# Kernel optimization log

Measured on AMD Instinct MI355X. Metric: run time of the kernel, lower is better.

The kernel has to match this reference:

```python
import jax, jax.numpy as jnp
import numpy as np

B, T, IN = 64, 64, 64      # batch, seq_len, input feature dim
C = 256                    # controller_size
N = 1024                   # memory_locations
MV = 64                    # memory_vector_size
OUT = 64                   # output_size
SHIFTS = (-1, 0, 1)        # maximum_shifts = 3 -> shifts -1,0,+1
EPS = 1e-8


def _glorot(key, shape):
    lim = np.sqrt(6.0 / (shape[0] + shape[1]))
    return jax.random.uniform(key, shape, jnp.float32, -lim, lim)


def setup_inputs() -> dict:
    key = jax.random.key(0)
    ks = jax.random.split(key, 8)
    x = jax.random.normal(ks[0], (B, T, IN), jnp.float32)
    # controller FC: input = concat(x_t, r_{t-1})
    Wc = _glorot(ks[1], (IN + MV, C)); bc = jnp.zeros((C,), jnp.float32)
    # read head emits k(MV), beta(1), g(1), s(3), gamma(1)
    Wr = _glorot(ks[2], (C, MV + 6)); br = jnp.zeros((MV + 6,), jnp.float32)
    # write head emits k, beta, g, s, gamma, e(MV), a(MV)
    Ww = _glorot(ks[3], (C, 3 * MV + 6)); bw = jnp.zeros((3 * MV + 6,), jnp.float32)
    # final FC: input = concat(controller_out, r_t)
    Wf = _glorot(ks[4], (C + MV, OUT)); bf = jnp.zeros((OUT,), jnp.float32)
    # state biases, as in NTM.__init__
    r_bias = 0.5 * jax.random.truncated_normal(ks[5], -2.0, 2.0, (1, MV)).astype(jnp.float32)
    w_bias = jax.nn.softmax(jax.random.normal(ks[6], (1, N), jnp.float32), axis=-1)
    M_bias = jnp.full((1, N, MV), 1e-6, jnp.float32)
    return {"x": x, "Wc": Wc, "bc": bc, "Wr": Wr, "br": br, "Ww": Ww, "bw": bw,
            "Wf": Wf, "bf": bf, "r_bias": r_bias, "w_bias": w_bias, "M_bias": M_bias}


def _head_params(h):
    # h: [B, MV+6] raw head projections
    k = jnp.tanh(h[:, :MV])                               # key [B,MV]
    beta = jax.nn.softplus(h[:, MV:MV + 1])               # key strength > 0
    g = jax.nn.sigmoid(h[:, MV + 1:MV + 2])               # interpolation gate
    s = jax.nn.softmax(h[:, MV + 2:MV + 5], axis=-1)      # shift weights [B,3]
    gamma = 1.0 + jax.nn.softplus(h[:, MV + 5:MV + 6])    # sharpening >= 1
    return k, beta, g, s, gamma


def _address(w_prev, M, k, beta, g, s, gamma):
    # content addressing: cosine similarity between key and memory rows
    dot = jnp.einsum('bnm,bm->bn', M, k)
    norms = jnp.linalg.norm(M, axis=-1) * jnp.linalg.norm(k, axis=-1, keepdims=True)
    w_c = jax.nn.softmax(beta * dot / (norms + EPS), axis=-1)
    # interpolation with previous weights
    w_g = g * w_c + (1.0 - g) * w_prev
    # circular convolution shift
    shifted = jnp.stack([jnp.roll(w_g, sh, axis=1) for sh in SHIFTS], axis=-1)  # [B,N,3]
    w_s = jnp.einsum('bns,bs->bn', shifted, s)
    # sharpening
    w_pow = (w_s + EPS) ** gamma
    return w_pow / jnp.sum(w_pow, axis=-1, keepdims=True)


def reference(x, Wc, bc, Wr, br, Ww, bw, Wf, bf, r_bias, w_bias, M_bias):
    b = x.shape[0]
    r0 = jnp.tile(r_bias, (b, 1))          # [B,MV]
    w0 = jnp.tile(w_bias, (b, 1))          # [B,N]
    M0 = jnp.tile(M_bias, (b, 1, 1))       # [B,N,MV]

    def step(carry, x_t):
        r, w, M = carry
        c = jnp.tanh(jnp.concatenate([x_t, r], axis=1) @ Wc + bc)   # controller [B,C]
        # write head: address, then erase + add memory update
        hw = c @ Ww + bw
        k, beta, g, s, gamma = _head_params(hw[:, :MV + 6])
        e = jax.nn.sigmoid(hw[:, MV + 6:2 * MV + 6])   # erase vector
        a = jnp.tanh(hw[:, 2 * MV + 6:])               # add vector
        w_w = _address(w, M, k, beta, g, s, gamma)     # [B,N]
        M = M * (1.0 - w_w[:, :, None] * e[:, None, :]) + w_w[:, :, None] * a[:, None, :]
        # read head: address (using write head's weights as previous), then read
        hr = c @ Wr + br
        w_r = _address(w_w, M, *_head_params(hr))
        r = jnp.einsum('bn,bnm->bm', w_r, M)           # read vector [B,MV]
        out = jax.nn.sigmoid(jnp.concatenate([c, r], axis=1) @ Wf + bf)
        return (r, w_r, M), out

    _, ys = jax.lax.scan(step, (r0, w0, M0), jnp.transpose(x, (1, 0, 2)))
    return jnp.transpose(ys, (1, 0, 2))  # [B,T,OUT]
```

## Files before the change

### kernel.cpp

```cpp
#include <hip/hip_runtime.h>
#include <hip/hip_bf16.h>
#include <math.h>


constexpr int kB  = 64;
constexpr int kT  = 64;
constexpr int kIN = 64;
constexpr int kC  = 256;
constexpr int kN  = 1024;
constexpr int kMV = 64;
constexpr int kOUT = 64;
constexpr int kHW = 198;
constexpr int kHR = 70;
constexpr int kHO = kHW + kHR;
constexpr int kHCP = 320;
constexpr int NT  = 512;
constexpr int NW  = NT / 64;
constexpr float kEPS = 1e-8f;

constexpr int kPWc = 0;
constexpr int kPHc = kPWc + kC * 128;
constexpr int kPWf = kPHc + kC * kHCP;
constexpr int kPTotal = kPWf + kOUT * (kC + kMV);
constexpr size_t kWsPack = 256 + (size_t)kPTotal * 4;
constexpr int kCpreElems = kB * kT * kC;
constexpr size_t kWsFull = kWsPack + (size_t)kCpreElems * 4;

__device__ __forceinline__ float ldf(const float* p, int i) { return p[i]; }
__device__ __forceinline__ float ldf(const __hip_bfloat16* p, int i) { return __bfloat162float(p[i]); }
__device__ __forceinline__ void stf(float* p, int i, float v) { p[i] = v; }
__device__ __forceinline__ void stf(__hip_bfloat16* p, int i, float v) { p[i] = __float2bfloat16(v); }

__device__ __forceinline__ void ld8(const __hip_bfloat16* p, float* f) {
  uint4 u = *reinterpret_cast<const uint4*>(p);
  f[0] = __uint_as_float(u.x << 16); f[1] = __uint_as_float(u.x & 0xffff0000u);
  f[2] = __uint_as_float(u.y << 16); f[3] = __uint_as_float(u.y & 0xffff0000u);
  f[4] = __uint_as_float(u.z << 16); f[5] = __uint_as_float(u.z & 0xffff0000u);
  f[6] = __uint_as_float(u.w << 16); f[7] = __uint_as_float(u.w & 0xffff0000u);
}
__device__ __forceinline__ void ld8(const float* p, float* f) {
  float4 a = reinterpret_cast<const float4*>(p)[0];
  float4 b = reinterpret_cast<const float4*>(p)[1];
  f[0] = a.x; f[1] = a.y; f[2] = a.z; f[3] = a.w;
  f[4] = b.x; f[5] = b.y; f[6] = b.z; f[7] = b.w;
}

__device__ __forceinline__ float fexp(float v) { return __expf(v); }
__device__ __forceinline__ float sigmoidf_(float v) {
  return __fdividef(1.f, 1.f + __expf(-v));
}
__device__ __forceinline__ float softplusf_(float v) {
  return v > 20.f ? v : __logf(1.f + __expf(v));
}
__device__ __forceinline__ float ftanh(float v) {
  float a = fminf(fabsf(v), 15.f);
  float e = __expf(2.f * a);
  float t = 1.f - __fdividef(2.f, e + 1.f);
  return v < 0.f ? -t : t;
}

__device__ __forceinline__ float wsum(float v) {
  v += __shfl_xor(v, 32); v += __shfl_xor(v, 16); v += __shfl_xor(v, 8);
  v += __shfl_xor(v, 4);  v += __shfl_xor(v, 2);  v += __shfl_xor(v, 1);
  return v;
}

template <typename TD>
__device__ __forceinline__ float dot64(const TD* row, const float* vec) {
  float a0 = 0.f, a1 = 0.f, a2 = 0.f, a3 = 0.f;
  #pragma unroll
  for (int q = 0; q < 8; ++q) {
    float f[8]; ld8(row + 8 * q, f);
    float4 va = *(const float4*)&vec[8 * q];
    float4 vb = *(const float4*)&vec[8 * q + 4];
    a0 = fmaf(va.x, f[0], a0); a1 = fmaf(va.y, f[1], a1);
    a2 = fmaf(va.z, f[2], a2); a3 = fmaf(va.w, f[3], a3);
    a0 = fmaf(vb.x, f[4], a0); a1 = fmaf(vb.y, f[5], a1);
    a2 = fmaf(vb.z, f[6], a2); a3 = fmaf(vb.w, f[7], a3);
  }
  return (a0 + a1) + (a2 + a3);
}

struct alignas(16) Smem {
  float M1s[16 * 512 * 4];
  float partA[1280];
  float E[kN];
  float WP[kN];
  float c[kC];
  float r[kMV];
  float k[kMV], kr[kMV], e[kMV], a[kMV];
  float bcS[kC], bwS[kHW], brS[kHR], bfS[kOUT];
  float red[2][NW];
  float scal[16];
};
static_assert(sizeof(Smem) <= 160 * 1024, "LDS budget");

__device__ __forceinline__ int m1idx(int blk, int row) { return (blk * 512 + row) * 4; }

__global__ void detect_dtype(const void* wb, int* flag) {
  const unsigned short* u = (const unsigned short*)wb;
  int lane = threadIdx.x;
  float s = 0.f;
  for (int i = lane; i < kN; i += 64)
    s += __uint_as_float(((unsigned int)u[i]) << 16);
  s = wsum(s);
  if (lane == 0 && blockIdx.x == 0)
    *flag = (s > 0.75f && s < 1.25f) ? 1 : 0;
}

template <typename TD, int WANT>
__global__ void repack_w(const TD* __restrict__ Wc, const TD* __restrict__ Ww,
                         const TD* __restrict__ Wr, const TD* __restrict__ Wf,
                         TD* __restrict__ pk, const int* __restrict__ flag) {
  if (*flag != WANT) return;
  for (int idx = blockIdx.x * blockDim.x + threadIdx.x; idx < kPTotal;
       idx += gridDim.x * blockDim.x) {
    TD v = (TD)0.0f;
    if (idx < kPHc) {
      int r = idx, j = r >> 7, i = r & 127;
      v = Wc[i * kC + j];
    } else if (idx < kPWf) {
      int r = idx - kPHc, i = r / kHCP, o = r - i * kHCP;
      if (o < kHW) v = Ww[i * kHW + o];
      else if (o < kHO) v = Wr[i * kHR + (o - kHW)];
    } else {
      int r = idx - kPWf, j = r / 320, i = r % 320;
      v = Wf[i * kOUT + j];
    }
    pk[idx] = v;
  }
}

template <typename TD, int WANT>
__global__ void cpre_kernel(const TD* __restrict__ x, const TD* __restrict__ bc,
                            const TD* __restrict__ pk, float* __restrict__ cpre,
                            const int* __restrict__ flag) {
  if (*flag != WANT) return;
  const int bt = blockIdx.x;
  const int tid = threadIdx.x;
  __shared__ float xs[kIN];
  if (tid < kIN) xs[tid] = ldf(x, (size_t)bt * kIN + tid);
  __syncthreads();
  const TD* row = pk + kPWc + tid * 128;
  float s = ldf(bc, tid) + dot64(row, xs);
  cpre[(size_t)bt * kC + tid] = s;
}

template <typename TD, int WANT, int MODE>
__global__ __launch_bounds__(NT, 1) void ntm_fused(
    const TD* __restrict__ x,
    const TD* __restrict__ Wc, const TD* __restrict__ bc,
    const TD* __restrict__ Wr, const TD* __restrict__ br,
    const TD* __restrict__ Ww, const TD* __restrict__ bw,
    const TD* __restrict__ Wf, const TD* __restrict__ bf,
    const TD* __restrict__ r_bias, const TD* __restrict__ w_bias,
    const TD* __restrict__ M_bias,
    const TD* __restrict__ pk, const float* __restrict__ cpre,
    TD* __restrict__ out, const int* __restrict__ flag) {
  if (*flag != WANT) return;
  __shared__ Smem sm;
  const int tid  = threadIdx.x;
  const int b    = blockIdx.x;
  const int lane = tid & 63;
  const int wid  = tid >> 6;

  if (tid < kC)  sm.bcS[tid] = ldf(bc, tid);
  if (tid < kHW) sm.bwS[tid] = ldf(bw, tid);
  if (tid < kHR) sm.brS[tid] = ldf(br, tid);
  if (tid < kOUT) sm.bfS[tid] = ldf(bf, tid);
  if (tid < kMV) sm.r[tid] = ldf(r_bias, tid);

  float M0[kMV];
  float n2_0 = 0.f, n2_1 = 0.f;
  #pragma unroll
  for (int jb = 0; jb < kMV; jb += 8) {
    float f0[8], f1[8];
    ld8(M_bias + (size_t)tid * kMV + jb, f0);
    ld8(M_bias + (size_t)(tid + NT) * kMV + jb, f1);
    #pragma unroll
    for (int u = 0; u < 8; ++u) {
      M0[jb + u] = f0[u];
      n2_0 = fmaf(f0[u], f0[u], n2_0);
      n2_1 = fmaf(f1[u], f1[u], n2_1);
    }
    *(float4*)&sm.M1s[m1idx(jb >> 2, tid)] = make_float4(f1[0], f1[1], f1[2], f1[3]);
    *(float4*)&sm.M1s[m1idx((jb >> 2) + 1, tid)] = make_float4(f1[4], f1[5], f1[6], f1[7]);
  }
  float wp0 = ldf(w_bias, tid);
  float wp1 = ldf(w_bias, tid + NT);
  __syncthreads();

  #pragma unroll 1
  for (int t = 0; t < kT; ++t) {
    if constexpr (MODE == 2) {
      if (tid < 256) {
        const int si = lane >> 3;
        const int g  = (wid << 3) + (lane & 7);
        const int obase = g * 8;
        float acc[8] = {0.f, 0.f, 0.f, 0.f, 0.f, 0.f, 0.f, 0.f};
        #pragma unroll
        for (int q = 0; q < 8; ++q) {
          int i = (q << 3) + si;
          float rv = sm.r[i];
          float f[8]; ld8(Wc + (kIN + i) * kC + obase, f);
          #pragma unroll
          for (int v = 0; v < 8; ++v) acc[v] = fmaf(rv, f[v], acc[v]);
        }
        #pragma unroll
        for (int v = 0; v < 8; ++v) {
          acc[v] += __shfl_xor(acc[v], 8);
          acc[v] += __shfl_xor(acc[v], 16);
          acc[v] += __shfl_xor(acc[v], 32);
        }
        if (si == 0) {
          const float* cp = &cpre[((size_t)b * kT + t) * kC + obase];
          float4 ca = *(const float4*)cp;
          float4 cb = *(const float4*)(cp + 4);
          sm.c[obase + 0] = ftanh(ca.x + acc[0]);
          sm.c[obase + 1] = ftanh(ca.y + acc[1]);
          sm.c[obase + 2] = ftanh(ca.z + acc[2]);
          sm.c[obase + 3] = ftanh(ca.w + acc[3]);
          sm.c[obase + 4] = ftanh(cb.x + acc[4]);
          sm.c[obase + 5] = ftanh(cb.y + acc[5]);
          sm.c[obase + 6] = ftanh(cb.z + acc[6]);
          sm.c[obase + 7] = ftanh(cb.w + acc[7]);
        }
      } else if (tid < 320 && t > 0) {
        const int j = tid - 256;
        float s = sm.bfS[j] + sm.partA[512 + j] + sm.partA[576 + j];
        s += dot64(pk + kPWf + j * (kC + kMV) + kC, sm.r);
        stf(out, ((size_t)b * kT + (t - 1)) * kOUT + j, sigmoidf_(s));
      }
    } else {
      if (tid < kC) {
        float s;
        if constexpr (MODE == 1) {
          s = sm.bcS[tid];
          const TD* xrow = x + ((size_t)b * kT + t) * kIN;
          const TD* row = pk + kPWc + tid * 128;
          #pragma unroll
          for (int q = 0; q < 8; ++q) {
            float f[8], xv[8];
            ld8(row + 8 * q, f); ld8(xrow + 8 * q, xv);
            #pragma unroll
            for (int u = 0; u < 8; ++u) s = fmaf(xv[u], f[u], s);
          }
          s += dot64(pk + kPWc + tid * 128 + 64, sm.r);
        } else {
          s = sm.bcS[tid];
          for (int i = 0; i < kIN; ++i)
            s = fmaf(ldf(x, ((size_t)b * kT + t) * kIN + i), ldf(Wc, i * kC + tid), s);
          for (int i = 0; i < kMV; ++i)
            s = fmaf(sm.r[i], ldf(Wc, (kIN + i) * kC + tid), s);
        }
        sm.c[tid] = ftanh(s);
      } else if (tid < 320 && t > 0) {
        const int j = tid - 256;
        float s = sm.bfS[j] + sm.partA[512 + j] + sm.partA[576 + j];
        if constexpr (MODE >= 1) {
          s += dot64(pk + kPWf + j * (kC + kMV) + kC, sm.r);
        } else {
          for (int i = 0; i < kMV; ++i)
            s = fmaf(sm.r[i], ldf(Wf, (kC + i) * kOUT + j), s);
        }
        stf(out, ((size_t)b * kT + (t - 1)) * kOUT + j, sigmoidf_(s));
      }
    }
    __syncthreads();

    if constexpr (MODE >= 1) {
      if (wid < 5) {
        const int si = lane >> 3;
        const int g  = (wid << 3) + (lane & 7);
        const int obase = g * 8;
        float acc[8] = {0.f, 0.f, 0.f, 0.f, 0.f, 0.f, 0.f, 0.f};
        #pragma unroll 4
        for (int q = 0; q < 32; ++q) {
          int i = (q << 3) + si;
          float cv = sm.c[i];
          float f[8]; ld8(pk + kPHc + i * kHCP + obase, f);
          #pragma unroll
          for (int v = 0; v < 8; ++v) acc[v] = fmaf(cv, f[v], acc[v]);
        }
        #pragma unroll
        for (int v = 0; v < 8; ++v) {
          acc[v] += __shfl_xor(acc[v], 8);
          acc[v] += __shfl_xor(acc[v], 16);
          acc[v] += __shfl_xor(acc[v], 32);
        }
        if (si == 0 && obase < kHO) {
          #pragma unroll
          for (int v = 0; v < 8; ++v)
            if (obase + v < kHO) sm.partA[obase + v] = acc[v];
        }
      }
    } else {
      if (tid < kHO) {
        float a0 = 0.f;
        for (int i = 0; i < kC; ++i) {
          float wv = (tid < kHW) ? ldf(Ww, i * kHW + tid)
                                 : ldf(Wr, i * kHR + (tid - kHW));
          a0 = fmaf(sm.c[i], wv, a0);
        }
        sm.partA[tid] = a0;
      }
    }
    __syncthreads();

    if (wid == 0) {
      float kv = ftanh(sm.partA[lane] + sm.bwS[lane]);
      sm.k[lane] = kv;
      float s = wsum(kv * kv);
      if (lane == 0) sm.scal[6] = sqrtf(s);
    } else if (wid == 1) {
      sm.e[lane] = sigmoidf_(sm.partA[70 + lane] + sm.bwS[70 + lane]);
    } else if (wid == 2) {
      sm.a[lane] = ftanh(sm.partA[134 + lane] + sm.bwS[134 + lane]);
    } else if (wid == 3) {
      float kv = ftanh(sm.partA[kHW + lane] + sm.brS[lane]);
      sm.kr[lane] = kv;
      float s = wsum(kv * kv);
      if (lane == 0) sm.scal[14] = sqrtf(s);
    } else if (wid == 4 || wid == 5) {
      const int si = lane >> 3;
      const int g  = lane & 7;
      const int obase = g * 8;
      const int ibase = (wid - 4) * 128;
      float acc[8] = {0.f, 0.f, 0.f, 0.f, 0.f, 0.f, 0.f, 0.f};
      #pragma unroll 4
      for (int q = 0; q < 16; ++q) {
        int i = ibase + (q << 3) + si;
        float cv = sm.c[i];
        float f[8]; ld8(Wf + i * kOUT + obase, f);
        #pragma unroll
        for (int v = 0; v < 8; ++v) acc[v] = fmaf(cv, f[v], acc[v]);
      }
      #pragma unroll
      for (int v = 0; v < 8; ++v) {
        acc[v] += __shfl_xor(acc[v], 8);
        acc[v] += __shfl_xor(acc[v], 16);
        acc[v] += __shfl_xor(acc[v], 32);
      }
      if (si == 0) {
        *(float4*)&sm.partA[512 + (wid - 4) * 64 + obase] =
            make_float4(acc[0], acc[1], acc[2], acc[3]);
        *(float4*)&sm.partA[512 + (wid - 4) * 64 + obase + 4] =
            make_float4(acc[4], acc[5], acc[6], acc[7]);
      }
    }
    __syncthreads();

    float ww0, ww1, gW, s0W, s1W, s2W, gammaW;
    float e0W, e1W, p0W, p1W;
    {
      float beta = softplusf_(sm.partA[64] + sm.bwS[64]);
      gW = sigmoidf_(sm.partA[65] + sm.bwS[65]);
      gammaW = 1.f + softplusf_(sm.partA[69] + sm.bwS[69]);
      float a0 = sm.partA[66] + sm.bwS[66];
      float a1 = sm.partA[67] + sm.bwS[67];
      float a2 = sm.partA[68] + sm.bwS[68];
      float mx = fmaxf(a0, fmaxf(a1, a2));
      float ex0 = fexp(a0 - mx), ex1 = fexp(a1 - mx), ex2 = fexp(a2 - mx);
      float dd = __fdividef(1.f, ex0 + ex1 + ex2);
      s0W = ex0 * dd; s1W = ex1 * dd; s2W = ex2 * dd;
      float kn = sm.scal[6];
      float d0a = 0.f, d0b = 0.f, d1a = 0.f, d1b = 0.f;
      #pragma unroll
      for (int bq = 0; bq < 16; ++bq) {
        float4 kv = *(const float4*)&sm.k[bq * 4];
        d0a = fmaf(M0[bq * 4],     kv.x, d0a);
        d0b = fmaf(M0[bq * 4 + 1], kv.y, d0b);
        d0a = fmaf(M0[bq * 4 + 2], kv.z, d0a);
        d0b = fmaf(M0[bq * 4 + 3], kv.w, d0b);
        float4 mv = *(const float4*)&sm.M1s[m1idx(bq, tid)];
        d1a = fmaf(mv.x, kv.x, d1a); d1b = fmaf(mv.y, kv.y, d1b);
        d1a = fmaf(mv.z, kv.z, d1a); d1b = fmaf(mv.w, kv.w, d1b);
      }
      float d0 = d0a + d0b, d1 = d1a + d1b;
      float sim0 = fminf(beta * d0 / (sqrtf(n2_0) * kn + kEPS), 80.f);
      float sim1 = fminf(beta * d1 / (sqrtf(n2_1) * kn + kEPS), 80.f);
      e0W = fexp(sim0); e1W = fexp(sim1);
      sm.E[tid] = e0W; sm.E[tid + NT] = e1W;
      sm.WP[tid] = wp0; sm.WP[tid + NT] = wp1;
      float sv = wsum(e0W + e1W);
      if (lane == 0) sm.red[0][wid] = sv;
    }
    __syncthreads();

    {
      float gsum = 0.f;
      #pragma unroll
      for (int i = 0; i < NW; ++i) gsum += sm.red[0][i];
      float inv = __fdividef(1.f, gsum);
      float wg0 = fmaf(gW, fmaf(e0W, inv, -wp0), wp0);
      float wg1 = fmaf(gW, fmaf(e1W, inv, -wp1), wp1);
      int np = (tid + 1) & (kN - 1), nm = (tid + kN - 1) & (kN - 1);
      float wgp = fmaf(gW, fmaf(sm.E[np], inv, -sm.WP[np]), sm.WP[np]);
      float wgm = fmaf(gW, fmaf(sm.E[nm], inv, -sm.WP[nm]), sm.WP[nm]);
      float ws0 = s0W * wgp + s1W * wg0 + s2W * wgm;
      int npb = (tid + NT + 1) & (kN - 1), nmb = (tid + NT - 1) & (kN - 1);
      float wgpb = fmaf(gW, fmaf(sm.E[npb], inv, -sm.WP[npb]), sm.WP[npb]);
      float wgmb = fmaf(gW, fmaf(sm.E[nmb], inv, -sm.WP[nmb]), sm.WP[nmb]);
      float ws1 = s0W * wgpb + s1W * wg1 + s2W * wgmb;
      p0W = fexp(gammaW * __logf(ws0 + kEPS));
      p1W = fexp(gammaW * __logf(ws1 + kEPS));
      float pv = wsum(p0W + p1W);
      if (lane == 0) sm.red[1][wid] = pv;
    }
    __syncthreads();
    {
      float psum = 0.f;
      #pragma unroll
      for (int i = 0; i < NW; ++i) psum += sm.red[1][i];
      float ipn = __fdividef(1.f, psum);
      ww0 = p0W * ipn; ww1 = p1W * ipn;
    }

    float gR, s0R, s1R, s2R, gammaR;
    float e0R, e1R, p0R, p1R;
    float dr0 = 0.f, dr1 = 0.f, nn0 = 0.f, nn1 = 0.f;
    {
      #pragma unroll
      for (int bq = 0; bq < 16; ++bq) {
        float4 ev = *(const float4*)&sm.e[bq * 4];
        float4 av = *(const float4*)&sm.a[bq * 4];
        float4 kv = *(const float4*)&sm.kr[bq * 4];
        {
          float m = fmaf(ww0, fmaf(-ev.x, M0[bq * 4], av.x), M0[bq * 4]);
          M0[bq * 4] = m; dr0 = fmaf(m, kv.x, dr0); nn0 = fmaf(m, m, nn0);
        }
        {
          float m = fmaf(ww0, fmaf(-ev.y, M0[bq * 4 + 1], av.y), M0[bq * 4 + 1]);
          M0[bq * 4 + 1] = m; dr0 = fmaf(m, kv.y, dr0); nn0 = fmaf(m, m, nn0);
        }
        {
          float m = fmaf(ww0, fmaf(-ev.z, M0[bq * 4 + 2], av.z), M0[bq * 4 + 2]);
          M0[bq * 4 + 2] = m; dr0 = fmaf(m, kv.z, dr0); nn0 = fmaf(m, m, nn0);
        }
        {
          float m = fmaf(ww0, fmaf(-ev.w, M0[bq * 4 + 3], av.w), M0[bq * 4 + 3]);
          M0[bq * 4 + 3] = m; dr0 = fmaf(m, kv.w, dr0); nn0 = fmaf(m, m, nn0);
        }
        int fi = m1idx(bq, tid);
        float4 mv = *(const float4*)&sm.M1s[fi];
        float4 nm;
        nm.x = fmaf(ww1, fmaf(-ev.x, mv.x, av.x), mv.x);
        dr1 = fmaf(nm.x, kv.x, dr1); nn1 = fmaf(nm.x, nm.x, nn1);
        nm.y = fmaf(ww1, fmaf(-ev.y, mv.y, av.y), mv.y);
        dr1 = fmaf(nm.y, kv.y, dr1); nn1 = fmaf(nm.y, nm.y, nn1);
        nm.z = fmaf(ww1, fmaf(-ev.z, mv.z, av.z), mv.z);
        dr1 = fmaf(nm.z, kv.z, dr1); nn1 = fmaf(nm.z, nm.z, nn1);
        nm.w = fmaf(ww1, fmaf(-ev.w, mv.w, av.w), mv.w);
        dr1 = fmaf(nm.w, kv.w, dr1); nn1 = fmaf(nm.w, nm.w, nn1);
        *(float4*)&sm.M1s[fi] = nm;
      }
      float beta = softplusf_(sm.partA[kHW + 64] + sm.brS[64]);
      gR = sigmoidf_(sm.partA[kHW + 65] + sm.brS[65]);
      gammaR = 1.f + softplusf_(sm.partA[kHW + 69] + sm.brS[69]);
      float a0 = sm.partA[kHW + 66] + sm.brS[66];
      float a1 = sm.partA[kHW + 67] + sm.brS[67];
      float a2 = sm.partA[kHW + 68] + sm.brS[68];
      float mx = fmaxf(a0, fmaxf(a1, a2));
      float ex0 = fexp(a0 - mx), ex1 = fexp(a1 - mx), ex2 = fexp(a2 - mx);
      float dd = __fdividef(1.f, ex0 + ex1 + ex2);
      s0R = ex0 * dd; s1R = ex1 * dd; s2R = ex2 * dd;
      float kn = sm.scal[14];
      float sim0 = fminf(beta * dr0 / (sqrtf(nn0) * kn + kEPS), 80.f);
      float sim1 = fminf(beta * dr1 / (sqrtf(nn1) * kn + kEPS), 80.f);
      e0R = fexp(sim0); e1R = fexp(sim1);
      sm.E[tid] = e0R; sm.E[tid + NT] = e1R;
      sm.WP[tid] = ww0; sm.WP[tid + NT] = ww1;
      float sv = wsum(e0R + e1R);
      if (lane == 0) sm.red[0][wid] = sv;
    }
    __syncthreads();

    {
      float gsum = 0.f;
      #pragma unroll
      for (int i = 0; i < NW; ++i) gsum += sm.red[0][i];
      float inv = __fdividef(1.f, gsum);
      float wg0 = fmaf(gR, fmaf(e0R, inv, -ww0), ww0);
      float wg1 = fmaf(gR, fmaf(e1R, inv, -ww1), ww1);
      int np = (tid + 1) & (kN - 1), nm = (tid + kN - 1) & (kN - 1);
      float wgp = fmaf(gR, fmaf(sm.E[np], inv, -sm.WP[np]), sm.WP[np]);
      float wgm = fmaf(gR, fmaf(sm.E[nm], inv, -sm.WP[nm]), sm.WP[nm]);
      float ws0 = s0R * wgp + s1R * wg0 + s2R * wgm;
      int npb = (tid + NT + 1) & (kN - 1), nmb = (tid + NT - 1) & (kN - 1);
      float wgpb = fmaf(gR, fmaf(sm.E[npb], inv, -sm.WP[npb]), sm.WP[npb]);
      float wgmb = fmaf(gR, fmaf(sm.E[nmb], inv, -sm.WP[nmb]), sm.WP[nmb]);
      float ws1 = s0R * wgpb + s1R * wg1 + s2R * wgmb;
      p0R = fexp(gammaR * __logf(ws0 + kEPS));
      p1R = fexp(gammaR * __logf(ws1 + kEPS));
      float pv = wsum(p0R + p1R);
      if (lane == 0) sm.red[1][wid] = pv;
      {
        float cur[16];
        const int b0 = lane & 1;
        #pragma unroll
        for (int qq = 0; qq < 8; ++qq) {
          float4 mv = *(const float4*)&sm.M1s[m1idx(qq, tid)];
          float v0 = fmaf(p0R, M0[4 * qq],     p1R * mv.x);
          float v1 = fmaf(p0R, M0[4 * qq + 1], p1R * mv.y);
          float keep = b0 ? v1 : v0, send = b0 ? v0 : v1;
          cur[2 * qq] = keep + __shfl_xor(send, 1);
          float v2 = fmaf(p0R, M0[4 * qq + 2], p1R * mv.z);
          float v3 = fmaf(p0R, M0[4 * qq + 3], p1R * mv.w);
          keep = b0 ? v3 : v2; send = b0 ? v2 : v3;
          cur[2 * qq + 1] = keep + __shfl_xor(send, 1);
        }
        #pragma unroll
        for (int st = 1; st < 5; ++st) {
          const int d = 1 << st;
          const int bb = (lane >> st) & 1;
          #pragma unroll
          for (int q = 0; q < (16 >> st); ++q) {
            float x0 = cur[2 * q], x1 = cur[2 * q + 1];
            float keep = bb ? x1 : x0, send = bb ? x0 : x1;
            cur[q] = keep + __shfl_xor(send, d);
          }
        }
        float tot = cur[0] + __shfl_xor(cur[0], 32);
        if (lane < 32) sm.partA[768 + wid * 64 + lane] = tot;
      }
      {
        float cur[16];
        const int b0 = lane & 1;
        #pragma unroll
        for (int qq = 0; qq < 8; ++qq) {
          float4 mv = *(const float4*)&sm.M1s[m1idx(8 + qq, tid)];
          float v0 = fmaf(p0R, M0[32 + 4 * qq],     p1R * mv.x);
          float v1 = fmaf(p0R, M0[32 + 4 * qq + 1], p1R * mv.y);
          float keep = b0 ? v1 : v0, send = b0 ? v0 : v1;
          cur[2 * qq] = keep + __shfl_xor(send, 1);
          float v2 = fmaf(p0R, M0[32 + 4 * qq + 2], p1R * mv.z);
          float v3 = fmaf(p0R, M0[32 + 4 * qq + 3], p1R * mv.w);
          keep = b0 ? v3 : v2; send = b0 ? v2 : v3;
          cur[2 * qq + 1] = keep + __shfl_xor(send, 1);
        }
        #pragma unroll
        for (int st = 1; st < 5; ++st) {
          const int d = 1 << st;
          const int bb = (lane >> st) & 1;
          #pragma unroll
          for (int q = 0; q < (16 >> st); ++q) {
            float x0 = cur[2 * q], x1 = cur[2 * q + 1];
            float keep = bb ? x1 : x0, send = bb ? x0 : x1;
            cur[q] = keep + __shfl_xor(send, d);
          }
        }
        float tot = cur[0] + __shfl_xor(cur[0], 32);
        if (lane < 32) sm.partA[768 + wid * 64 + 32 + lane] = tot;
      }
    }
    __syncthreads();

    {
      float psum = 0.f;
      #pragma unroll
      for (int i = 0; i < NW; ++i) psum += sm.red[1][i];
      float ipn = __fdividef(1.f, psum);
      wp0 = p0R * ipn; wp1 = p1R * ipn;
      n2_0 = nn0; n2_1 = nn1;
      if (tid < kMV) {
        float s = sm.partA[768 + tid];
        #pragma unroll
        for (int w = 1; w < NW; ++w) s += sm.partA[768 + w * 64 + tid];
        sm.r[tid] = s * ipn;
      }
    }
    __syncthreads();
  }

  if (tid >= 256 && tid < 320) {
    const int j = tid - 256;
    float s = sm.bfS[j] + sm.partA[512 + j] + sm.partA[576 + j];
    if constexpr (MODE >= 1) {
      s += dot64(pk + kPWf + j * (kC + kMV) + kC, sm.r);
    } else {
      for (int i = 0; i < kMV; ++i)
        s = fmaf(sm.r[i], ldf(Wf, (kC + i) * kOUT + j), s);
    }
    stf(out, ((size_t)b * kT + (kT - 1)) * kOUT + j, sigmoidf_(s));
  }
}

template <typename TD, int WANT, int MODE>
static void launch_variant(void* const* d_in, void* d_out, const int* flag,
                           const void* pk, const float* cpre, hipStream_t stream) {
  ntm_fused<TD, WANT, MODE><<<dim3(kB), dim3(NT), 0, stream>>>(
      (const TD*)d_in[0], (const TD*)d_in[1], (const TD*)d_in[2],
      (const TD*)d_in[3], (const TD*)d_in[4], (const TD*)d_in[5],
      (const TD*)d_in[6], (const TD*)d_in[7], (const TD*)d_in[8],
      (const TD*)d_in[9], (const TD*)d_in[10], (const TD*)d_in[11],
      (const TD*)pk, cpre, (TD*)d_out, flag);
}

extern "C" void kernel_launch(void* const* d_in, const int* in_sizes, int n_in,
                              void* d_out, int out_size, void* d_ws, size_t ws_size,
                              hipStream_t stream) {
  (void)in_sizes; (void)n_in; (void)out_size;
  int* flag = (int*)d_ws;
  detect_dtype<<<dim3(1), dim3(64), 0, stream>>>(d_in[10], flag);
  if (ws_size >= kWsPack) {
    void* pk = (void*)((char*)d_ws + 256);
    repack_w<__hip_bfloat16, 1><<<dim3(256), dim3(256), 0, stream>>>(
        (const __hip_bfloat16*)d_in[1], (const __hip_bfloat16*)d_in[5],
        (const __hip_bfloat16*)d_in[3], (const __hip_bfloat16*)d_in[7],
        (__hip_bfloat16*)pk, flag);
    repack_w<float, 0><<<dim3(256), dim3(256), 0, stream>>>(
        (const float*)d_in[1], (const float*)d_in[5],
        (const float*)d_in[3], (const float*)d_in[7],
        (float*)pk, flag);
    if (ws_size >= kWsFull) {
      float* cpre = (float*)((char*)d_ws + kWsPack);
      cpre_kernel<__hip_bfloat16, 1><<<dim3(kB * kT), dim3(kC), 0, stream>>>(
          (const __hip_bfloat16*)d_in[0], (const __hip_bfloat16*)d_in[2],
          (const __hip_bfloat16*)pk, cpre, flag);
      cpre_kernel<float, 0><<<dim3(kB * kT), dim3(kC), 0, stream>>>(
          (const float*)d_in[0], (const float*)d_in[2],
          (const float*)pk, cpre, flag);
      launch_variant<__hip_bfloat16, 1, 2>(d_in, d_out, flag, pk, cpre, stream);
      launch_variant<float, 0, 2>(d_in, d_out, flag, pk, cpre, stream);
    } else {
      launch_variant<__hip_bfloat16, 1, 1>(d_in, d_out, flag, pk, nullptr, stream);
      launch_variant<float, 0, 1>(d_in, d_out, flag, pk, nullptr, stream);
    }
  } else {
    launch_variant<__hip_bfloat16, 1, 0>(d_in, d_out, flag, nullptr, nullptr, stream);
    launch_variant<float, 0, 0>(d_in, d_out, flag, nullptr, nullptr, stream);
  }
}
```

Before: 1.010 ms.

## Repack weights as fp32 and move Wf controller projection into head-GEMM phase

The packed weight buffer is now always fp32 and gains two new row-major copies: the recurrent part of Wc and the controller part of Wf. The per-step recurrent controller matvec and the Wf·c projection read from these packed copies instead of the raw inputs. The Wf·c projection moves from two warps in a later phase to a single warp (wid 5) running alongside the head GEMM, which removes one partial-sum add. In exchange the packed buffer is larger, bf16 inputs are read at double the bytes, and one warp now does twice the Wf work.

Measured after the change: 979.7 us. 1.03x faster.

```diff
diff --git a/kernel.cpp b/kernel.cpp
--- a/kernel.cpp
+++ b/kernel.cpp
@@ -18,10 +18,12 @@
 constexpr int NW  = NT / 64;
 constexpr float kEPS = 1e-8f;
 
-constexpr int kPWc = 0;
-constexpr int kPHc = kPWc + kC * 128;
-constexpr int kPWf = kPHc + kC * kHCP;
-constexpr int kPTotal = kPWf + kOUT * (kC + kMV);
+constexpr int kPWcT = 0;
+constexpr int kPHc  = kPWcT + kC * 128;
+constexpr int kPWfT = kPHc + kC * kHCP;
+constexpr int kPWcR = kPWfT + kOUT * (kC + kMV);
+constexpr int kPWfR = kPWcR + kMV * kC;
+constexpr int kPTotal = kPWfR + kC * kOUT;
 constexpr size_t kWsPack = 256 + (size_t)kPTotal * 4;
 constexpr int kCpreElems = kB * kT * kC;
 constexpr size_t kWsFull = kWsPack + (size_t)kCpreElems * 4;
@@ -111,21 +113,27 @@
 template <typename TD, int WANT>
 __global__ void repack_w(const TD* __restrict__ Wc, const TD* __restrict__ Ww,
                          const TD* __restrict__ Wr, const TD* __restrict__ Wf,
-                         TD* __restrict__ pk, const int* __restrict__ flag) {
+                         float* __restrict__ pk, const int* __restrict__ flag) {
   if (*flag != WANT) return;
   for (int idx = blockIdx.x * blockDim.x + threadIdx.x; idx < kPTotal;
        idx += gridDim.x * blockDim.x) {
-    TD v = (TD)0.0f;
+    float v = 0.0f;
     if (idx < kPHc) {
       int r = idx, j = r >> 7, i = r & 127;
-      v = Wc[i * kC + j];
-    } else if (idx < kPWf) {
+      v = ldf(Wc, i * kC + j);
+    } else if (idx < kPWfT) {
       int r = idx - kPHc, i = r / kHCP, o = r - i * kHCP;
-      if (o < kHW) v = Ww[i * kHW + o];
-      else if (o < kHO) v = Wr[i * kHR + (o - kHW)];
+      if (o < kHW) v = ldf(Ww, i * kHW + o);
+      else if (o < kHO) v = ldf(Wr, i * kHR + (o - kHW));
+    } else if (idx < kPWcR) {
+      int r = idx - kPWfT, j = r / 320, i = r % 320;
+      v = ldf(Wf, i * kOUT + j);
+    } else if (idx < kPWfR) {
+      int r = idx - kPWcR, i = r >> 8, j = r & 255;
+      v = ldf(Wc, (kIN + i) * kC + j);
     } else {
-      int r = idx - kPWf, j = r / 320, i = r % 320;
-      v = Wf[i * kOUT + j];
+      int r = idx - kPWfR, i = r >> 6, j = r & 63;
+      v = ldf(Wf, i * kOUT + j);
     }
     pk[idx] = v;
   }
@@ -133,7 +141,7 @@
 
 template <typename TD, int WANT>
 __global__ void cpre_kernel(const TD* __restrict__ x, const TD* __restrict__ bc,
-                            const TD* __restrict__ pk, float* __restrict__ cpre,
+                            const float* __restrict__ pk, float* __restrict__ cpre,
                             const int* __restrict__ flag) {
   if (*flag != WANT) return;
   const int bt = blockIdx.x;
@@ -141,7 +149,7 @@
   __shared__ float xs[kIN];
   if (tid < kIN) xs[tid] = ldf(x, (size_t)bt * kIN + tid);
   __syncthreads();
-  const TD* row = pk + kPWc + tid * 128;
+  const float* row = pk + kPWcT + tid * 128;
   float s = ldf(bc, tid) + dot64(row, xs);
   cpre[(size_t)bt * kC + tid] = s;
 }
@@ -155,7 +163,7 @@
     const TD* __restrict__ Wf, const TD* __restrict__ bf,
     const TD* __restrict__ r_bias, const TD* __restrict__ w_bias,
     const TD* __restrict__ M_bias,
-    const TD* __restrict__ pk, const float* __restrict__ cpre,
+    const float* __restrict__ pk, const float* __restrict__ cpre,
     TD* __restrict__ out, const int* __restrict__ flag) {
   if (*flag != WANT) return;
   __shared__ Smem sm;
@@ -202,7 +210,7 @@
         for (int q = 0; q < 8; ++q) {
           int i = (q << 3) + si;
           float rv = sm.r[i];
-          float f[8]; ld8(Wc + (kIN + i) * kC + obase, f);
+          float f[8]; ld8(pk + kPWcR + i * kC + obase, f);
           #pragma unroll
           for (int v = 0; v < 8; ++v) acc[v] = fmaf(rv, f[v], acc[v]);
         }
@@ -227,8 +235,8 @@
         }
       } else if (tid < 320 && t > 0) {
         const int j = tid - 256;
-        float s = sm.bfS[j] + sm.partA[512 + j] + sm.partA[576 + j];
-        s += dot64(pk + kPWf + j * (kC + kMV) + kC, sm.r);
+        float s = sm.bfS[j] + sm.partA[512 + j];
+        s += dot64(pk + kPWfT + j * (kC + kMV) + kC, sm.r);
         stf(out, ((size_t)b * kT + (t - 1)) * kOUT + j, sigmoidf_(s));
       }
     } else {
@@ -237,7 +245,7 @@
         if constexpr (MODE == 1) {
           s = sm.bcS[tid];
           const TD* xrow = x + ((size_t)b * kT + t) * kIN;
-          const TD* row = pk + kPWc + tid * 128;
+          const float* row = pk + kPWcT + tid * 128;
           #pragma unroll
           for (int q = 0; q < 8; ++q) {
             float f[8], xv[8];
@@ -245,7 +253,7 @@
             #pragma unroll
             for (int u = 0; u < 8; ++u) s = fmaf(xv[u], f[u], s);
           }
-          s += dot64(pk + kPWc + tid * 128 + 64, sm.r);
+          s += dot64(pk + kPWcT + tid * 128 + 64, sm.r);
         } else {
           s = sm.bcS[tid];
           for (int i = 0; i < kIN; ++i)
@@ -256,9 +264,9 @@
         sm.c[tid] = ftanh(s);
       } else if (tid < 320 && t > 0) {
         const int j = tid - 256;
-        float s = sm.bfS[j] + sm.partA[512 + j] + sm.partA[576 + j];
-        if constexpr (MODE >= 1) {
-          s += dot64(pk + kPWf + j * (kC + kMV) + kC, sm.r);
+        float s = sm.bfS[j] + sm.partA[512 + j];
+        if constexpr (MODE == 1) {
+          s += dot64(pk + kPWfT + j * (kC + kMV) + kC, sm.r);
         } else {
           for (int i = 0; i < kMV; ++i)
             s = fmaf(sm.r[i], ldf(Wf, (kC + i) * kOUT + j), s);
@@ -293,6 +301,31 @@
           for (int v = 0; v < 8; ++v)
             if (obase + v < kHO) sm.partA[obase + v] = acc[v];
         }
+      } else if (wid == 5) {
+        const int si = lane >> 3;
+        const int g  = lane & 7;
+        const int obase = g * 8;
+        float acc[8] = {0.f, 0.f, 0.f, 0.f, 0.f, 0.f, 0.f, 0.f};
+        #pragma unroll 4
+        for (int q = 0; q < 32; ++q) {
+          int i = (q << 3) + si;
+          float cv = sm.c[i];
+          float f[8]; ld8(pk + kPWfR + i * kOUT + obase, f);
+          #pragma unroll
+          for (int v = 0; v < 8; ++v) acc[v] = fmaf(cv, f[v], acc[v]);
+        }
+        #pragma unroll
+        for (int v = 0; v < 8; ++v) {
+          acc[v] += __shfl_xor(acc[v], 8);
+          acc[v] += __shfl_xor(acc[v], 16);
+          acc[v] += __shfl_xor(acc[v], 32);
+        }
+        if (si == 0) {
+          *(float4*)&sm.partA[512 + obase] =
+              make_float4(acc[0], acc[1], acc[2], acc[3]);
+          *(float4*)&sm.partA[512 + obase + 4] =
+              make_float4(acc[4], acc[5], acc[6], acc[7]);
+        }
       }
     } else {
       if (tid < kHO) {
@@ -303,6 +336,28 @@
           a0 = fmaf(sm.c[i], wv, a0);
         }
         sm.partA[tid] = a0;
+      } else if (wid == 5) {
+        const int si = lane >> 3;
+        const int g  = lane & 7;
+        const int obase = g * 8;
+        float acc[8] = {0.f, 0.f, 0.f, 0.f, 0.f, 0.f, 0.f, 0.f};
+        for (int q = 0; q < 32; ++q) {
+          int i = (q << 3) + si;
+          float cv = sm.c[i];
+          #pragma unroll
+          for (int v = 0; v < 8; ++v)
+            acc[v] = fmaf(cv, ldf(Wf, i * kOUT + obase + v), acc[v]);
+        }
+        #pragma unroll
+        for (int v = 0; v < 8; ++v) {
+          acc[v] += __shfl_xor(acc[v], 8);
+          acc[v] += __shfl_xor(acc[v], 16);
+          acc[v] += __shfl_xor(acc[v], 32);
+        }
+        if (si == 0) {
+          #pragma unroll
+          for (int v = 0; v < 8; ++v) sm.partA[512 + obase + v] = acc[v];
+        }
       }
     }
     __syncthreads();
@@ -321,32 +376,6 @@
       sm.kr[lane] = kv;
       float s = wsum(kv * kv);
       if (lane == 0) sm.scal[14] = sqrtf(s);
-    } else if (wid == 4 || wid == 5) {
-      const int si = lane >> 3;
-      const int g  = lane & 7;
-      const int obase = g * 8;
-      const int ibase = (wid - 4) * 128;
-      float acc[8] = {0.f, 0.f, 0.f, 0.f, 0.f, 0.f, 0.f, 0.f};
-      #pragma unroll 4
-      for (int q = 0; q < 16; ++q) {
-        int i = ibase + (q << 3) + si;
-        float cv = sm.c[i];
-        float f[8]; ld8(Wf + i * kOUT + obase, f);
-        #pragma unroll
-        for (int v = 0; v < 8; ++v) acc[v] = fmaf(cv, f[v], acc[v]);
-      }
-      #pragma unroll
-      for (int v = 0; v < 8; ++v) {
-        acc[v] += __shfl_xor(acc[v], 8);
-        acc[v] += __shfl_xor(acc[v], 16);
-        acc[v] += __shfl_xor(acc[v], 32);
-      }
-      if (si == 0) {
-        *(float4*)&sm.partA[512 + (wid - 4) * 64 + obase] =
-            make_float4(acc[0], acc[1], acc[2], acc[3]);
-        *(float4*)&sm.partA[512 + (wid - 4) * 64 + obase + 4] =
-            make_float4(acc[4], acc[5], acc[6], acc[7]);
-      }
     }
     __syncthreads();
 
@@ -574,9 +603,9 @@
 
   if (tid >= 256 && tid < 320) {
     const int j = tid - 256;
-    float s = sm.bfS[j] + sm.partA[512 + j] + sm.partA[576 + j];
+    float s = sm.bfS[j] + sm.partA[512 + j];
     if constexpr (MODE >= 1) {
-      s += dot64(pk + kPWf + j * (kC + kMV) + kC, sm.r);
+      s += dot64(pk + kPWfT + j * (kC + kMV) + kC, sm.r);
     } else {
       for (int i = 0; i < kMV; ++i)
         s = fmaf(sm.r[i], ldf(Wf, (kC + i) * kOUT + j), s);
@@ -587,13 +616,13 @@
 
 template <typename TD, int WANT, int MODE>
 static void launch_variant(void* const* d_in, void* d_out, const int* flag,
-                           const void* pk, const float* cpre, hipStream_t stream) {
+                           const float* pk, const float* cpre, hipStream_t stream) {
   ntm_fused<TD, WANT, MODE><<<dim3(kB), dim3(NT), 0, stream>>>(
       (const TD*)d_in[0], (const TD*)d_in[1], (const TD*)d_in[2],
       (const TD*)d_in[3], (const TD*)d_in[4], (const TD*)d_in[5],
       (const TD*)d_in[6], (const TD*)d_in[7], (const TD*)d_in[8],
       (const TD*)d_in[9], (const TD*)d_in[10], (const TD*)d_in[11],
-      (const TD*)pk, cpre, (TD*)d_out, flag);
+      pk, cpre, (TD*)d_out, flag);
 }
 
 extern "C" void kernel_launch(void* const* d_in, const int* in_sizes, int n_in,
@@ -603,23 +632,23 @@
   int* flag = (int*)d_ws;
   detect_dtype<<<dim3(1), dim3(64), 0, stream>>>(d_in[10], flag);
   if (ws_size >= kWsPack) {
-    void* pk = (void*)((char*)d_ws + 256);
+    float* pk = (float*)((char*)d_ws + 256);
     repack_w<__hip_bfloat16, 1><<<dim3(256), dim3(256), 0, stream>>>(
         (const __hip_bfloat16*)d_in[1], (const __hip_bfloat16*)d_in[5],
         (const __hip_bfloat16*)d_in[3], (const __hip_bfloat16*)d_in[7],
-        (__hip_bfloat16*)pk, flag);
+        pk, flag);
     repack_w<float, 0><<<dim3(256), dim3(256), 0, stream>>>(
         (const float*)d_in[1], (const float*)d_in[5],
         (const float*)d_in[3], (const float*)d_in[7],
-        (float*)pk, flag);
+        pk, flag);
     if (ws_size >= kWsFull) {
       float* cpre = (float*)((char*)d_ws + kWsPack);
       cpre_kernel<__hip_bfloat16, 1><<<dim3(kB * kT), dim3(kC), 0, stream>>>(
           (const __hip_bfloat16*)d_in[0], (const __hip_bfloat16*)d_in[2],
-          (const __hip_bfloat16*)pk, cpre, flag);
+          pk, cpre, flag);
       cpre_kernel<float, 0><<<dim3(kB * kT), dim3(kC), 0, stream>>>(
           (const float*)d_in[0], (const float*)d_in[2],
-          (const float*)pk, cpre, flag);
+          pk, cpre, flag);
       launch_variant<__hip_bfloat16, 1, 2>(d_in, d_out, flag, pk, cpre, stream);
       launch_variant<float, 0, 2>(d_in, d_out, flag, pk, cpre, stream);
     } else {
```
